# Kernel tuning notes

Hardware: AMD Instinct MI355X
Metric: run time of the kernel (lower is better)

The kernel has to match this reference:

```python
import jax, jax.numpy as jnp
import numpy as np

GROUPS = 16
EPS = 1e-5


def _dcn_v2(x, offset, mask, weight):
    """Modulated deformable 3x3 conv, stride=1, pad=1, no bias.
    x: [B,C,H,W], offset: [B,18,H,W] (dy,dx interleaved per kernel point),
    mask: [B,9,H,W] (modulation scalars), weight: [O,C,3,3]."""
    B, C, H, W = x.shape
    O = weight.shape[0]
    K = 9
    # kernel-point displacements, row-major (kh, kw): k = kh*3 + kw
    ky = jnp.repeat(jnp.arange(3) - 1, 3).astype(x.dtype)   # [9]
    kx = jnp.tile(jnp.arange(3) - 1, 3).astype(x.dtype)      # [9]
    dy = offset[:, 0::2]  # [B,9,H,W]
    dx = offset[:, 1::2]  # [B,9,H,W]
    hh = jnp.arange(H, dtype=x.dtype)
    ww = jnp.arange(W, dtype=x.dtype)
    # sampling coordinates (stride=1, pad=1)
    ys = hh[None, None, :, None] + ky[None, :, None, None] + dy  # [B,9,H,W]
    xs = ww[None, None, None, :] + kx[None, :, None, None] + dx  # [B,9,H,W]

    y0 = jnp.floor(ys)
    x0 = jnp.floor(xs)
    wy1 = ys - y0
    wx1 = xs - x0
    y0i = y0.astype(jnp.int32)
    x0i = x0.astype(jnp.int32)

    flat = x.reshape(B, C, H * W)

    def gather(yi, xi, w):
        # yi, xi, w: [B,9,H,W]; zero-padding outside the image
        valid = (yi >= 0) & (yi < H) & (xi >= 0) & (xi < W)
        idx = jnp.clip(yi, 0, H - 1) * W + jnp.clip(xi, 0, W - 1)  # [B,9,H,W]
        g = jnp.take_along_axis(flat, idx.reshape(B, 1, K * H * W), axis=2)
        g = g.reshape(B, C, K, H, W)
        return g * (w * valid.astype(x.dtype))[:, None]  # [B,C,9,H,W]

    val = (gather(y0i,     x0i,     (1 - wy1) * (1 - wx1))
         + gather(y0i,     x0i + 1, (1 - wy1) * wx1)
         + gather(y0i + 1, x0i,     wy1 * (1 - wx1))
         + gather(y0i + 1, x0i + 1, wy1 * wx1))
    val = val * mask[:, None]  # modulation
    # implicit GEMM: [B,C,9,H,W] x [O,C,9] -> [B,O,H,W]
    return jnp.einsum('bckhw,ock->bohw', val, weight.reshape(O, C, K))


def _group_norm(x, gamma, beta):
    B, C, H, W = x.shape
    xg = x.reshape(B, GROUPS, C // GROUPS, H, W)
    mu = xg.mean(axis=(2, 3, 4), keepdims=True)
    var = xg.var(axis=(2, 3, 4), keepdims=True)
    xn = ((xg - mu) * jax.lax.rsqrt(var + EPS)).reshape(B, C, H, W)
    return xn * gamma[None, :, None, None] + beta[None, :, None, None]


def setup_inputs() -> dict:
    key = jax.random.key(0)
    k1, k2, k3, k4 = jax.random.split(key, 4)
    B, C, O, H, W = 8, 256, 256, 64, 64
    x = jax.random.normal(k1, (B, C, H, W), dtype=jnp.float32)
    offset = jax.random.normal(k2, (B, 18, H, W), dtype=jnp.float32)
    mask = jax.random.uniform(k3, (B, 9, H, W), dtype=jnp.float32)
    weight = jax.random.normal(k4, (O, C, 3, 3), dtype=jnp.float32) * (1.0 / np.sqrt(C * 9))
    gamma = jnp.ones((O,), dtype=jnp.float32)
    beta = jnp.zeros((O,), dtype=jnp.float32)
    return {"x": x, "offset": offset, "mask": mask, "weight": weight,
            "gamma": gamma, "beta": beta}


def reference(x, offset, mask, weight, gamma, beta):
    out = _dcn_v2(x, offset, mask, weight)
    return _group_norm(out, gamma, beta)
```

## Files before the change

kernel.cpp:

```cpp
#include <hip/hip_runtime.h>
#include <stdint.h>


#define B_ 8
#define C_ 256
#define O_ 256
#define H_ 64
#define W_ 64
#define HW_ 4096
#define KTOT 2304
#define GROUPS_ 16
#define EPS_ 1e-5f
#define NSTEP 36
#define VROW 72

typedef float  f32x4  __attribute__((ext_vector_type(4)));
typedef short  short8 __attribute__((ext_vector_type(8)));
typedef unsigned int   u32;
typedef unsigned short u16;

#define XT_BYTES   (B_*HW_*C_*2)
#define WIMG_OFF   XT_BYTES
#define WIMG_BYTES (72*16*64*16)
#define STATS_OFF  (WIMG_OFF + WIMG_BYTES)

__device__ __forceinline__ u32 bf16r(float f) {
    u32 u = __float_as_uint(f);
    return (u + 0x7fffu + ((u >> 16) & 1u)) >> 16;
}
__device__ __forceinline__ u32 pack_bf16x2(float lo, float hi) {
    return bf16r(lo) | (bf16r(hi) << 16);
}
__device__ __forceinline__ u32 pack_perm(float lo, float hi) {
    return __builtin_amdgcn_perm(__float_as_uint(hi), __float_as_uint(lo), 0x07060302u);
}
__device__ __forceinline__ float bflo(u32 u) { return __uint_as_float(u << 16); }
__device__ __forceinline__ float bfhi_f(u32 u) { return __uint_as_float(u); }

__device__ __forceinline__ void barrier_lds() {
    asm volatile("s_waitcnt lgkmcnt(0)\n\ts_barrier" ::: "memory");
}

__global__ void k_prep(const float* __restrict__ x, u16* __restrict__ xt,
                       const float* __restrict__ w, u16* __restrict__ wimg) {
    const int bid = blockIdx.x;
    const int tid = threadIdx.x;
    if (bid < 2048) {
        __shared__ float tile[64][65];
        const int b = bid >> 8, ct = (bid >> 6) & 3, pt = bid & 63;
#pragma unroll
        for (int pass = 0; pass < 4; ++pass) {
            const int r  = (tid >> 4) + pass * 16;
            const int pq = tid & 15;
            const f32x4 v = *(const f32x4*)&x[(((size_t)(b * C_ + ct * 64 + r)) << 12)
                                              + pt * 64 + pq * 4];
            tile[r][pq * 4 + 0] = v.x;
            tile[r][pq * 4 + 1] = v.y;
            tile[r][pq * 4 + 2] = v.z;
            tile[r][pq * 4 + 3] = v.w;
        }
        __syncthreads();
        const int pr = tid >> 2, cg = tid & 3;
        u32 o[8];
#pragma unroll
        for (int j = 0; j < 8; ++j)
            o[j] = pack_bf16x2(tile[cg * 16 + 2 * j][pr], tile[cg * 16 + 2 * j + 1][pr]);
        u16* dst = &xt[(((size_t)b << 12) + pt * 64 + pr) * 256 + ct * 64 + cg * 16];
        *(uint4*)dst       = *(uint4*)&o[0];
        *(uint4*)(dst + 8) = *(uint4*)&o[4];
    } else {
        const int item = (bid - 2048) * 256 + tid;
        if (item < 72 * 1024) {
            const int sub = item >> 10;
            const int idx = item & 1023;
            const int k  = sub >> 3;
            const int c0 = (sub & 7) * 32;
            const int lane = idx & 63;
            const int frag = idx >> 6;
            const int col = lane & 15, quad = lane >> 4;
            const int n = frag * 16 + col;
            const float* src = w + (size_t)n * KTOT + (size_t)(c0 + quad * 8) * 9 + k;
            u32 o[4];
#pragma unroll
            for (int j = 0; j < 4; ++j)
                o[j] = pack_bf16x2(src[(size_t)(2 * j) * 9], src[(size_t)(2 * j + 1) * 9]);
            *(uint4*)&wimg[((size_t)sub * 1024 + idx) * 8] = *(uint4*)o;
        }
    }
}

__device__ __forceinline__ void issue_gather(const u16* __restrict__ cb,
                                             const float* __restrict__ mwp,
                                             const int* __restrict__ mip,
                                             int gpos, uint4 g[8], f32x4& mw) {
    mw = *(const f32x4*)&mwp[gpos * 4];
    const int4 ix = *(const int4*)&mip[gpos * 4];
    const u16* p0 = cb + ix.x;
    const u16* p1 = cb + ix.y;
    const u16* p2 = cb + ix.z;
    const u16* p3 = cb + ix.w;
    g[0] = *(const uint4*)p0; g[1] = *(const uint4*)(p0 + 8);
    g[2] = *(const uint4*)p1; g[3] = *(const uint4*)(p1 + 8);
    g[4] = *(const uint4*)p2; g[5] = *(const uint4*)(p2 + 8);
    g[6] = *(const uint4*)p3; g[7] = *(const uint4*)(p3 + 8);
}

__device__ __forceinline__ void interp_store(const uint4 g[8], f32x4 mw, u16* dst) {
    float s[16];
#pragma unroll
    for (int i = 0; i < 16; ++i) s[i] = 0.f;
    const float ww[4] = {mw.x, mw.y, mw.z, mw.w};
#pragma unroll
    for (int cr = 0; cr < 4; ++cr) {
        const float wg = ww[cr];
        const uint4 a = g[2 * cr], bq = g[2 * cr + 1];
        s[0]  += wg * bflo(a.x);  s[1]  += wg * bfhi_f(a.x);
        s[2]  += wg * bflo(a.y);  s[3]  += wg * bfhi_f(a.y);
        s[4]  += wg * bflo(a.z);  s[5]  += wg * bfhi_f(a.z);
        s[6]  += wg * bflo(a.w);  s[7]  += wg * bfhi_f(a.w);
        s[8]  += wg * bflo(bq.x); s[9]  += wg * bfhi_f(bq.x);
        s[10] += wg * bflo(bq.y); s[11] += wg * bfhi_f(bq.y);
        s[12] += wg * bflo(bq.z); s[13] += wg * bfhi_f(bq.z);
        s[14] += wg * bflo(bq.w); s[15] += wg * bfhi_f(bq.w);
    }
    uint4 pk0, pk1;
    pk0.x = pack_perm(s[0], s[1]);   pk0.y = pack_perm(s[2], s[3]);
    pk0.z = pack_perm(s[4], s[5]);   pk0.w = pack_perm(s[6], s[7]);
    pk1.x = pack_perm(s[8], s[9]);   pk1.y = pack_perm(s[10], s[11]);
    pk1.z = pack_perm(s[12], s[13]); pk1.w = pack_perm(s[14], s[15]);
    *(uint4*)dst = pk0;
    *(uint4*)(dst + 8) = pk1;
}

__device__ __forceinline__ void load_wfrags(const u16* __restrict__ wimg, int s,
                                            int wid, int lane, short8 bf[8]) {
#pragma unroll
    for (int kc = 0; kc < 2; ++kc)
#pragma unroll
        for (int ni = 0; ni < 4; ++ni)
            bf[kc * 4 + ni] = *(const short8*)
                &wimg[(((size_t)(2 * s + kc) * 16 + wid * 4 + ni) * 64 + lane) * 8];
}

__launch_bounds__(256, 2)
__global__ void k_dcn(const u16* __restrict__ xt, const u16* __restrict__ wimg,
                      const float* __restrict__ offp, const float* __restrict__ mskp,
                      float* __restrict__ out, float* __restrict__ stats) {
    __shared__ __align__(16) float meta_w[9 * 64 * 4];
    __shared__ __align__(16) int   meta_i[9 * 64 * 4];
    __shared__ __align__(16) u16   lds_v[2][64 * VROW];

    const int tid = threadIdx.x;
    const int gid = blockIdx.x;
    const int b   = gid & 7;
    const int m0  = (gid >> 3) * 64;
    const int lane = tid & 63, wid = tid >> 6;
    const int col = lane & 15, quad = lane >> 4;
    const int gpos = tid >> 2, oct = tid & 3;

    const u16* xtb = xt + ((size_t)b << 20);

    for (int it = tid; it < 576; it += 256) {
        const int pos = it & 63, k = it >> 6;
        const int pg = m0 + pos;
        const int hh = pg >> 6, wwi = pg & 63;
        const float dy = offp[((size_t)(b * 18 + 2 * k) << 12) + pg];
        const float dx = offp[((size_t)(b * 18 + 2 * k + 1) << 12) + pg];
        const float mv = mskp[((size_t)(b * 9 + k) << 12) + pg];
        const float ys = (float)(hh + (k / 3) - 1) + dy;
        const float xs = (float)(wwi + (k % 3) - 1) + dx;
        const float y0f = floorf(ys), x0f = floorf(xs);
        const int y0 = (int)y0f, x0 = (int)x0f;
        const float wy1 = ys - y0f, wx1 = xs - x0f;
        const float wy0 = 1.f - wy1, wx0 = 1.f - wx1;
        const int y1 = y0 + 1, x1 = x0 + 1;
        const float vy0 = (y0 >= 0 && y0 < H_) ? 1.f : 0.f;
        const float vy1 = (y1 >= 0 && y1 < H_) ? 1.f : 0.f;
        const float vx0 = (x0 >= 0 && x0 < W_) ? 1.f : 0.f;
        const float vx1 = (x1 >= 0 && x1 < W_) ? 1.f : 0.f;
        const int y0c = min(max(y0, 0), H_ - 1), y1c = min(max(y1, 0), H_ - 1);
        const int x0c = min(max(x0, 0), W_ - 1), x1c = min(max(x1, 0), W_ - 1);
        meta_w[it * 4 + 0] = mv * wy0 * wx0 * vy0 * vx0;
        meta_w[it * 4 + 1] = mv * wy0 * wx1 * vy0 * vx1;
        meta_w[it * 4 + 2] = mv * wy1 * wx0 * vy1 * vx0;
        meta_w[it * 4 + 3] = mv * wy1 * wx1 * vy1 * vx1;
        meta_i[it * 4 + 0] = (y0c * W_ + x0c) << 8;
        meta_i[it * 4 + 1] = (y0c * W_ + x1c) << 8;
        meta_i[it * 4 + 2] = (y1c * W_ + x0c) << 8;
        meta_i[it * 4 + 3] = (y1c * W_ + x1c) << 8;
    }
    __syncthreads();

    uint4 g2[2][8]; f32x4 mw2[2]; short8 bf_cur[8], bf_nxt[8];
    issue_gather(xtb + 0 + oct * 16, &meta_w[0], &meta_i[0], gpos, g2[0], mw2[0]);
    load_wfrags(wimg, 0, wid, lane, bf_cur);
    interp_store(g2[0], mw2[0], &lds_v[0][gpos * VROW + oct * 16]);
    issue_gather(xtb + 64 + oct * 16, &meta_w[0], &meta_i[0], gpos, g2[1], mw2[1]);
    __syncthreads();

    f32x4 acc[4][4];
#pragma unroll
    for (int i = 0; i < 4; ++i)
#pragma unroll
        for (int j = 0; j < 4; ++j) acc[i][j] = (f32x4){0.f, 0.f, 0.f, 0.f};

#pragma unroll 2
    for (int s = 0; s < NSTEP; ++s) {
        const int p = s & 1;

        if (s + 1 < NSTEP) load_wfrags(wimg, s + 1, wid, lane, bf_nxt);

        if (s + 2 < NSTEP) {
            const int sn = s + 2;
            const int kn = sn >> 2, c0n = (sn & 3) * 64;
            issue_gather(xtb + c0n + oct * 16, &meta_w[kn * 256], &meta_i[kn * 256],
                         gpos, g2[p], mw2[p]);
        }

#pragma unroll
        for (int kc = 0; kc < 2; ++kc) {
            short8 af[4];
#pragma unroll
            for (int mi = 0; mi < 4; ++mi)
                af[mi] = *(const short8*)
                    &lds_v[p][(mi * 16 + col) * VROW + kc * 32 + quad * 8];
#pragma unroll
            for (int mi = 0; mi < 4; ++mi)
#pragma unroll
                for (int ni = 0; ni < 4; ++ni)
                    acc[mi][ni] = __builtin_amdgcn_mfma_f32_16x16x32_bf16(
                        af[mi], bf_cur[kc * 4 + ni], acc[mi][ni], 0, 0, 0);
        }

        if (s + 1 < NSTEP)
            interp_store(g2[1 - p], mw2[1 - p], &lds_v[1 - p][gpos * VROW + oct * 16]);

        barrier_lds();

#pragma unroll
        for (int j = 0; j < 8; ++j) bf_cur[j] = bf_nxt[j];
    }

#pragma unroll
    for (int mi = 0; mi < 4; ++mi)
#pragma unroll
        for (int ni = 0; ni < 4; ++ni) {
            const int o  = wid * 64 + ni * 16 + col;
            const int pg = m0 + mi * 16 + quad * 4;
            *(f32x4*)(out + (((size_t)b * O_ + o) << 12) + pg) = acc[mi][ni];
        }

#pragma unroll
    for (int ni = 0; ni < 4; ++ni) {
        float s = 0.f, s2 = 0.f;
#pragma unroll
        for (int mi = 0; mi < 4; ++mi) {
            f32x4 v = acc[mi][ni];
            s  += v.x + v.y + v.z + v.w;
            s2 += v.x * v.x + v.y * v.y + v.z * v.z + v.w * v.w;
        }
#pragma unroll
        for (int d = 32; d > 0; d >>= 1) {
            s  += __shfl_xor(s, d, 64);
            s2 += __shfl_xor(s2, d, 64);
        }
        if (lane == 0) {
            const int gI = wid * 4 + ni;
            atomicAdd(&stats[b * GROUPS_ + gI], s);
            atomicAdd(&stats[128 + b * GROUPS_ + gI], s2);
        }
    }
}

__global__ void k_gn(float* __restrict__ out, const float* __restrict__ stats,
                     const float* __restrict__ gamma, const float* __restrict__ beta) {
    const int blk = blockIdx.x;
    const int b = blk >> 8, o = blk & 255;
    const int gI = b * GROUPS_ + (o >> 4);
    const float n = 65536.f;
    const float mean = stats[gI] / n;
    const float var  = stats[128 + gI] / n - mean * mean;
    const float inv  = rsqrtf(fmaxf(var, 0.f) + EPS_);
    const float scale = inv * gamma[o];
    const float shift = beta[o] - mean * scale;
    f32x4* p = (f32x4*)(out + ((size_t)blk << 12));
    const int t = threadIdx.x;
#pragma unroll
    for (int i = 0; i < 4; ++i) {
        f32x4 v = p[t + i * 256];
        p[t + i * 256] = v * scale + shift;
    }
}

extern "C" void kernel_launch(void* const* d_in, const int* in_sizes, int n_in,
                              void* d_out, int out_size, void* d_ws, size_t ws_size,
                              hipStream_t stream) {
    const float* x     = (const float*)d_in[0];
    const float* offp  = (const float*)d_in[1];
    const float* mskp  = (const float*)d_in[2];
    const float* w     = (const float*)d_in[3];
    const float* gamma = (const float*)d_in[4];
    const float* beta  = (const float*)d_in[5];
    float* outp = (float*)d_out;

    u16*   xt    = (u16*)d_ws;
    u16*   wimg  = (u16*)((char*)d_ws + WIMG_OFF);
    float* stats = (float*)((char*)d_ws + STATS_OFF);

    hipMemsetAsync(stats, 0, 1024, stream);
    k_prep<<<dim3(2048 + 288), dim3(256), 0, stream>>>(x, xt, w, wimg);
    k_dcn<<<dim3(512), dim3(256), 0, stream>>>(xt, wimg, offp, mskp, outp, stats);
    k_gn<<<dim3(2048), dim3(256), 0, stream>>>(outp, stats, gamma, beta);
}
```

Before: 185.0 us.

## Double k_dcn block to 512 threads, halve per-thread gather and MFMA work

The DCN kernel now runs 8 waves per block instead of 4. Each wave owns 32 output channels instead of 64, and each thread gathers 8 channels per bilinear corner instead of 16. Weight-fragment prefetching into a second register set is removed, so fragments load at the start of each step, which cuts register pressure so more waves can stay resident to hide gather latency. The separate memset of the statistics buffer is folded into an extra block of the prep kernel, saving one launch. In exchange, weight-load latency is no longer hidden behind the previous step, and the block pays more barrier cost.

Result: faster. 181.2 us (-2.1%).

```diff
diff --git a/kernel.cpp b/kernel.cpp
--- a/kernel.cpp
+++ b/kernel.cpp
@@ -42,9 +42,14 @@
 }
 
 __global__ void k_prep(const float* __restrict__ x, u16* __restrict__ xt,
-                       const float* __restrict__ w, u16* __restrict__ wimg) {
+                       const float* __restrict__ w, u16* __restrict__ wimg,
+                       float* __restrict__ stats) {
     const int bid = blockIdx.x;
     const int tid = threadIdx.x;
+    if (bid >= 2048 + 288) {
+        stats[tid] = 0.f;
+        return;
+    }
     if (bid < 2048) {
         __shared__ float tile[64][65];
         const int b = bid >> 8, ct = (bid >> 6) & 3, pt = bid & 63;
@@ -92,57 +97,48 @@
 __device__ __forceinline__ void issue_gather(const u16* __restrict__ cb,
                                              const float* __restrict__ mwp,
                                              const int* __restrict__ mip,
-                                             int gpos, uint4 g[8], f32x4& mw) {
+                                             int gpos, uint4 g[4], f32x4& mw) {
     mw = *(const f32x4*)&mwp[gpos * 4];
     const int4 ix = *(const int4*)&mip[gpos * 4];
-    const u16* p0 = cb + ix.x;
-    const u16* p1 = cb + ix.y;
-    const u16* p2 = cb + ix.z;
-    const u16* p3 = cb + ix.w;
-    g[0] = *(const uint4*)p0; g[1] = *(const uint4*)(p0 + 8);
-    g[2] = *(const uint4*)p1; g[3] = *(const uint4*)(p1 + 8);
-    g[4] = *(const uint4*)p2; g[5] = *(const uint4*)(p2 + 8);
-    g[6] = *(const uint4*)p3; g[7] = *(const uint4*)(p3 + 8);
-}
-
-__device__ __forceinline__ void interp_store(const uint4 g[8], f32x4 mw, u16* dst) {
-    float s[16];
-#pragma unroll
-    for (int i = 0; i < 16; ++i) s[i] = 0.f;
+    g[0] = *(const uint4*)(cb + ix.x);
+    g[1] = *(const uint4*)(cb + ix.y);
+    g[2] = *(const uint4*)(cb + ix.z);
+    g[3] = *(const uint4*)(cb + ix.w);
+}
+
+__device__ __forceinline__ void interp_store(const uint4 g[4], f32x4 mw, u16* dst) {
+    float s[8];
+#pragma unroll
+    for (int i = 0; i < 8; ++i) s[i] = 0.f;
     const float ww[4] = {mw.x, mw.y, mw.z, mw.w};
 #pragma unroll
     for (int cr = 0; cr < 4; ++cr) {
         const float wg = ww[cr];
-        const uint4 a = g[2 * cr], bq = g[2 * cr + 1];
-        s[0]  += wg * bflo(a.x);  s[1]  += wg * bfhi_f(a.x);
-        s[2]  += wg * bflo(a.y);  s[3]  += wg * bfhi_f(a.y);
-        s[4]  += wg * bflo(a.z);  s[5]  += wg * bfhi_f(a.z);
-        s[6]  += wg * bflo(a.w);  s[7]  += wg * bfhi_f(a.w);
-        s[8]  += wg * bflo(bq.x); s[9]  += wg * bfhi_f(bq.x);
-        s[10] += wg * bflo(bq.y); s[11] += wg * bfhi_f(bq.y);
-        s[12] += wg * bflo(bq.z); s[13] += wg * bfhi_f(bq.z);
-        s[14] += wg * bflo(bq.w); s[15] += wg * bfhi_f(bq.w);
-    }
-    uint4 pk0, pk1;
-    pk0.x = pack_perm(s[0], s[1]);   pk0.y = pack_perm(s[2], s[3]);
-    pk0.z = pack_perm(s[4], s[5]);   pk0.w = pack_perm(s[6], s[7]);
-    pk1.x = pack_perm(s[8], s[9]);   pk1.y = pack_perm(s[10], s[11]);
-    pk1.z = pack_perm(s[12], s[13]); pk1.w = pack_perm(s[14], s[15]);
-    *(uint4*)dst = pk0;
-    *(uint4*)(dst + 8) = pk1;
+        const uint4 a = g[cr];
+        s[0] += wg * bflo(a.x);  s[1] += wg * bfhi_f(a.x);
+        s[2] += wg * bflo(a.y);  s[3] += wg * bfhi_f(a.y);
+        s[4] += wg * bflo(a.z);  s[5] += wg * bfhi_f(a.z);
+        s[6] += wg * bflo(a.w);  s[7] += wg * bfhi_f(a.w);
+    }
+    uint4 pk;
+    pk.x = pack_perm(s[0], s[1]);
+    pk.y = pack_perm(s[2], s[3]);
+    pk.z = pack_perm(s[4], s[5]);
+    pk.w = pack_perm(s[6], s[7]);
+    *(uint4*)dst = pk;
 }
 
 __device__ __forceinline__ void load_wfrags(const u16* __restrict__ wimg, int s,
-                                            int wid, int lane, short8 bf[8]) {
+                                            int wid, int lane, short8 bf[4]) {
 #pragma unroll
     for (int kc = 0; kc < 2; ++kc)
 #pragma unroll
-        for (int ni = 0; ni < 4; ++ni)
-            bf[kc * 4 + ni] = *(const short8*)
-                &wimg[(((size_t)(2 * s + kc) * 16 + wid * 4 + ni) * 64 + lane) * 8];
-}
-
-__launch_bounds__(256, 2)
+        for (int ni = 0; ni < 2; ++ni)
+            bf[kc * 2 + ni] = *(const short8*)
+                &wimg[(((size_t)(2 * s + kc) * 16 + wid * 2 + ni) * 64 + lane) * 8];
+}
+
+__launch_bounds__(512, 4)
 __global__ void k_dcn(const u16* __restrict__ xt, const u16* __restrict__ wimg,
                       const float* __restrict__ offp, const float* __restrict__ mskp,
                       float* __restrict__ out, float* __restrict__ stats) {
@@ -156,11 +152,11 @@
     const int m0  = (gid >> 3) * 64;
     const int lane = tid & 63, wid = tid >> 6;
     const int col = lane & 15, quad = lane >> 4;
-    const int gpos = tid >> 2, oct = tid & 3;
+    const int gpos = tid >> 3, slot = tid & 7;
 
     const u16* xtb = xt + ((size_t)b << 20);
 
-    for (int it = tid; it < 576; it += 256) {
+    for (int it = tid; it < 576; it += 512) {
         const int pos = it & 63, k = it >> 6;
         const int pg = m0 + pos;
         const int hh = pg >> 6, wwi = pg & 63;
@@ -191,29 +187,28 @@
     }
     __syncthreads();
 
-    uint4 g2[2][8]; f32x4 mw2[2]; short8 bf_cur[8], bf_nxt[8];
-    issue_gather(xtb + 0 + oct * 16, &meta_w[0], &meta_i[0], gpos, g2[0], mw2[0]);
-    load_wfrags(wimg, 0, wid, lane, bf_cur);
-    interp_store(g2[0], mw2[0], &lds_v[0][gpos * VROW + oct * 16]);
-    issue_gather(xtb + 64 + oct * 16, &meta_w[0], &meta_i[0], gpos, g2[1], mw2[1]);
+    uint4 g2[2][4]; f32x4 mw2[2]; short8 bf[4];
+    issue_gather(xtb + 0 + slot * 8, &meta_w[0], &meta_i[0], gpos, g2[0], mw2[0]);
+    interp_store(g2[0], mw2[0], &lds_v[0][gpos * VROW + slot * 8]);
+    issue_gather(xtb + 64 + slot * 8, &meta_w[0], &meta_i[0], gpos, g2[1], mw2[1]);
     __syncthreads();
 
-    f32x4 acc[4][4];
+    f32x4 acc[4][2];
 #pragma unroll
     for (int i = 0; i < 4; ++i)
 #pragma unroll
-        for (int j = 0; j < 4; ++j) acc[i][j] = (f32x4){0.f, 0.f, 0.f, 0.f};
+        for (int j = 0; j < 2; ++j) acc[i][j] = (f32x4){0.f, 0.f, 0.f, 0.f};
 
 #pragma unroll 2
     for (int s = 0; s < NSTEP; ++s) {
         const int p = s & 1;
 
-        if (s + 1 < NSTEP) load_wfrags(wimg, s + 1, wid, lane, bf_nxt);
+        load_wfrags(wimg, s, wid, lane, bf);
 
         if (s + 2 < NSTEP) {
             const int sn = s + 2;
             const int kn = sn >> 2, c0n = (sn & 3) * 64;
-            issue_gather(xtb + c0n + oct * 16, &meta_w[kn * 256], &meta_i[kn * 256],
+            issue_gather(xtb + c0n + slot * 8, &meta_w[kn * 256], &meta_i[kn * 256],
                          gpos, g2[p], mw2[p]);
         }
 
@@ -227,31 +222,28 @@
 #pragma unroll
             for (int mi = 0; mi < 4; ++mi)
 #pragma unroll
-                for (int ni = 0; ni < 4; ++ni)
+                for (int ni = 0; ni < 2; ++ni)
                     acc[mi][ni] = __builtin_amdgcn_mfma_f32_16x16x32_bf16(
-                        af[mi], bf_cur[kc * 4 + ni], acc[mi][ni], 0, 0, 0);
+                        af[mi], bf[kc * 2 + ni], acc[mi][ni], 0, 0, 0);
         }
 
         if (s + 1 < NSTEP)
-            interp_store(g2[1 - p], mw2[1 - p], &lds_v[1 - p][gpos * VROW + oct * 16]);
+            interp_store(g2[1 - p], mw2[1 - p], &lds_v[1 - p][gpos * VROW + slot * 8]);
 
         barrier_lds();
-
-#pragma unroll
-        for (int j = 0; j < 8; ++j) bf_cur[j] = bf_nxt[j];
     }
 
 #pragma unroll
     for (int mi = 0; mi < 4; ++mi)
 #pragma unroll
-        for (int ni = 0; ni < 4; ++ni) {
-            const int o  = wid * 64 + ni * 16 + col;
+        for (int ni = 0; ni < 2; ++ni) {
+            const int o  = wid * 32 + ni * 16 + col;
             const int pg = m0 + mi * 16 + quad * 4;
             *(f32x4*)(out + (((size_t)b * O_ + o) << 12) + pg) = acc[mi][ni];
         }
 
 #pragma unroll
-    for (int ni = 0; ni < 4; ++ni) {
+    for (int ni = 0; ni < 2; ++ni) {
         float s = 0.f, s2 = 0.f;
 #pragma unroll
         for (int mi = 0; mi < 4; ++mi) {
@@ -265,7 +257,7 @@
             s2 += __shfl_xor(s2, d, 64);
         }
         if (lane == 0) {
-            const int gI = wid * 4 + ni;
+            const int gI = wid * 2 + ni;
             atomicAdd(&stats[b * GROUPS_ + gI], s);
             atomicAdd(&stats[128 + b * GROUPS_ + gI], s2);
         }
@@ -307,8 +299,7 @@
     u16*   wimg  = (u16*)((char*)d_ws + WIMG_OFF);
     float* stats = (float*)((char*)d_ws + STATS_OFF);
 
-    hipMemsetAsync(stats, 0, 1024, stream);
-    k_prep<<<dim3(2048 + 288), dim3(256), 0, stream>>>(x, xt, w, wimg);
-    k_dcn<<<dim3(512), dim3(256), 0, stream>>>(xt, wimg, offp, mskp, outp, stats);
+    k_prep<<<dim3(2048 + 288 + 1), dim3(256), 0, stream>>>(x, xt, w, wimg, stats);
+    k_dcn<<<dim3(512), dim3(512), 0, stream>>>(xt, wimg, offp, mskp, outp, stats);
     k_gn<<<dim3(2048), dim3(256), 0, stream>>>(outp, stats, gamma, beta);
 }
```

## Split DCN block into producer gather waves and consumer MFMA waves

Applied to the files above, without the earlier changes.

The DCN kernel now launches 512 threads per block. Four waves only gather and bilinearly interpolate samples into the double-buffered LDS tile, while the other four waves load weight fragments and run the MFMA accumulation. This warp specialization is meant to overlap the irregular gather latency with matrix math, in exchange for per-step barriers across twice as many waves and losing the weight-fragment prefetch. Separately, the stats memset is folded into an extra block of the prep kernel to drop one launch.

Result: slower. 222.8 us (+20.4%).

```diff
diff --git a/kernel.cpp b/kernel.cpp
--- a/kernel.cpp
+++ b/kernel.cpp
@@ -42,9 +42,14 @@
 }
 
 __global__ void k_prep(const float* __restrict__ x, u16* __restrict__ xt,
-                       const float* __restrict__ w, u16* __restrict__ wimg) {
+                       const float* __restrict__ w, u16* __restrict__ wimg,
+                       float* __restrict__ stats) {
     const int bid = blockIdx.x;
     const int tid = threadIdx.x;
+    if (bid >= 2048 + 288) {
+        stats[tid] = 0.f;
+        return;
+    }
     if (bid < 2048) {
         __shared__ float tile[64][65];
         const int b = bid >> 8, ct = (bid >> 6) & 3, pt = bid & 63;
@@ -89,12 +94,12 @@
     }
 }
 
-__device__ __forceinline__ void issue_gather(const u16* __restrict__ cb,
-                                             const float* __restrict__ mwp,
-                                             const int* __restrict__ mip,
-                                             int gpos, uint4 g[8], f32x4& mw) {
-    mw = *(const f32x4*)&mwp[gpos * 4];
-    const int4 ix = *(const int4*)&mip[gpos * 4];
+__device__ __forceinline__ void issue_gather16(const u16* __restrict__ cb,
+                                               const float* __restrict__ mwp,
+                                               const int* __restrict__ mip,
+                                               int ppos, uint4 g[8], f32x4& mw) {
+    mw = *(const f32x4*)&mwp[ppos * 4];
+    const int4 ix = *(const int4*)&mip[ppos * 4];
     const u16* p0 = cb + ix.x;
     const u16* p1 = cb + ix.y;
     const u16* p2 = cb + ix.z;
@@ -105,7 +110,7 @@
     g[6] = *(const uint4*)p3; g[7] = *(const uint4*)(p3 + 8);
 }
 
-__device__ __forceinline__ void interp_store(const uint4 g[8], f32x4 mw, u16* dst) {
+__device__ __forceinline__ void interp_store16(const uint4 g[8], f32x4 mw, u16* dst) {
     float s[16];
 #pragma unroll
     for (int i = 0; i < 16; ++i) s[i] = 0.f;
@@ -132,17 +137,7 @@
     *(uint4*)(dst + 8) = pk1;
 }
 
-__device__ __forceinline__ void load_wfrags(const u16* __restrict__ wimg, int s,
-                                            int wid, int lane, short8 bf[8]) {
-#pragma unroll
-    for (int kc = 0; kc < 2; ++kc)
-#pragma unroll
-        for (int ni = 0; ni < 4; ++ni)
-            bf[kc * 4 + ni] = *(const short8*)
-                &wimg[(((size_t)(2 * s + kc) * 16 + wid * 4 + ni) * 64 + lane) * 8];
-}
-
-__launch_bounds__(256, 2)
+__launch_bounds__(512, 2)
 __global__ void k_dcn(const u16* __restrict__ xt, const u16* __restrict__ wimg,
                       const float* __restrict__ offp, const float* __restrict__ mskp,
                       float* __restrict__ out, float* __restrict__ stats) {
@@ -155,12 +150,11 @@
     const int b   = gid & 7;
     const int m0  = (gid >> 3) * 64;
     const int lane = tid & 63, wid = tid >> 6;
-    const int col = lane & 15, quad = lane >> 4;
-    const int gpos = tid >> 2, oct = tid & 3;
+    const bool producer = (wid < 4);
 
     const u16* xtb = xt + ((size_t)b << 20);
 
-    for (int it = tid; it < 576; it += 256) {
+    for (int it = tid; it < 576; it += 512) {
         const int pos = it & 63, k = it >> 6;
         const int pg = m0 + pos;
         const int hh = pg >> 6, wwi = pg & 63;
@@ -191,82 +185,93 @@
     }
     __syncthreads();
 
-    uint4 g2[2][8]; f32x4 mw2[2]; short8 bf_cur[8], bf_nxt[8];
-    issue_gather(xtb + 0 + oct * 16, &meta_w[0], &meta_i[0], gpos, g2[0], mw2[0]);
-    load_wfrags(wimg, 0, wid, lane, bf_cur);
-    interp_store(g2[0], mw2[0], &lds_v[0][gpos * VROW + oct * 16]);
-    issue_gather(xtb + 64 + oct * 16, &meta_w[0], &meta_i[0], gpos, g2[1], mw2[1]);
+    const int ppos = tid >> 2, pslot = tid & 3;
+    const u16* gb = xtb + pslot * 16;
+    u16* wdst0 = &lds_v[0][ppos * VROW + pslot * 16];
+    u16* wdst1 = &lds_v[1][ppos * VROW + pslot * 16];
+    uint4 g2[2][8]; f32x4 mw2[2];
+    const int cw = wid - 4;
+    const int col = lane & 15, quad = lane >> 4;
+    f32x4 acc[4][4];
+
+    if (producer) {
+        issue_gather16(gb, &meta_w[0], &meta_i[0], ppos, g2[0], mw2[0]);
+        interp_store16(g2[0], mw2[0], wdst0);
+        issue_gather16(gb + 64, &meta_w[0], &meta_i[0], ppos, g2[1], mw2[1]);
+    } else {
+#pragma unroll
+        for (int i = 0; i < 4; ++i)
+#pragma unroll
+            for (int j = 0; j < 4; ++j) acc[i][j] = (f32x4){0.f, 0.f, 0.f, 0.f};
+    }
     __syncthreads();
-
-    f32x4 acc[4][4];
-#pragma unroll
-    for (int i = 0; i < 4; ++i)
-#pragma unroll
-        for (int j = 0; j < 4; ++j) acc[i][j] = (f32x4){0.f, 0.f, 0.f, 0.f};
 
 #pragma unroll 2
     for (int s = 0; s < NSTEP; ++s) {
-        const int p = s & 1;
-
-        if (s + 1 < NSTEP) load_wfrags(wimg, s + 1, wid, lane, bf_nxt);
-
-        if (s + 2 < NSTEP) {
-            const int sn = s + 2;
-            const int kn = sn >> 2, c0n = (sn & 3) * 64;
-            issue_gather(xtb + c0n + oct * 16, &meta_w[kn * 256], &meta_i[kn * 256],
-                         gpos, g2[p], mw2[p]);
-        }
-
-#pragma unroll
-        for (int kc = 0; kc < 2; ++kc) {
-            short8 af[4];
-#pragma unroll
-            for (int mi = 0; mi < 4; ++mi)
-                af[mi] = *(const short8*)
-                    &lds_v[p][(mi * 16 + col) * VROW + kc * 32 + quad * 8];
-#pragma unroll
-            for (int mi = 0; mi < 4; ++mi)
+        if (producer) {
+            if (s + 2 < NSTEP) {
+                const int sn = s + 2;
+                issue_gather16(gb + (sn & 3) * 64,
+                               &meta_w[(sn >> 2) * 256], &meta_i[(sn >> 2) * 256],
+                               ppos, g2[s & 1], mw2[s & 1]);
+            }
+            if (s + 1 < NSTEP)
+                interp_store16(g2[(s + 1) & 1], mw2[(s + 1) & 1],
+                               ((s + 1) & 1) ? wdst1 : wdst0);
+        } else {
+            short8 bf[8];
+#pragma unroll
+            for (int kc = 0; kc < 2; ++kc)
 #pragma unroll
                 for (int ni = 0; ni < 4; ++ni)
-                    acc[mi][ni] = __builtin_amdgcn_mfma_f32_16x16x32_bf16(
-                        af[mi], bf_cur[kc * 4 + ni], acc[mi][ni], 0, 0, 0);
-        }
-
-        if (s + 1 < NSTEP)
-            interp_store(g2[1 - p], mw2[1 - p], &lds_v[1 - p][gpos * VROW + oct * 16]);
-
-        barrier_lds();
-
-#pragma unroll
-        for (int j = 0; j < 8; ++j) bf_cur[j] = bf_nxt[j];
-    }
+                    bf[kc * 4 + ni] = *(const short8*)
+                        &wimg[(((size_t)(2 * s + kc) * 16 + cw * 4 + ni) * 64 + lane) * 8];
+#pragma unroll
+            for (int kc = 0; kc < 2; ++kc) {
+                short8 af[4];
+#pragma unroll
+                for (int mi = 0; mi < 4; ++mi)
+                    af[mi] = *(const short8*)
+                        &lds_v[s & 1][(mi * 16 + col) * VROW + kc * 32 + quad * 8];
+#pragma unroll
+                for (int mi = 0; mi < 4; ++mi)
+#pragma unroll
+                    for (int ni = 0; ni < 4; ++ni)
+                        acc[mi][ni] = __builtin_amdgcn_mfma_f32_16x16x32_bf16(
+                            af[mi], bf[kc * 4 + ni], acc[mi][ni], 0, 0, 0);
+            }
+        }
+        if (s + 1 < NSTEP) barrier_lds();
+    }
+
+    if (producer) return;
 
 #pragma unroll
     for (int mi = 0; mi < 4; ++mi)
 #pragma unroll
         for (int ni = 0; ni < 4; ++ni) {
-            const int o  = wid * 64 + ni * 16 + col;
+            const int o  = cw * 64 + ni * 16 + col;
             const int pg = m0 + mi * 16 + quad * 4;
             *(f32x4*)(out + (((size_t)b * O_ + o) << 12) + pg) = acc[mi][ni];
         }
 
 #pragma unroll
     for (int ni = 0; ni < 4; ++ni) {
-        float s = 0.f, s2 = 0.f;
+        float s1 = 0.f, s2 = 0.f;
 #pragma unroll
         for (int mi = 0; mi < 4; ++mi) {
             f32x4 v = acc[mi][ni];
-            s  += v.x + v.y + v.z + v.w;
+            s1 += v.x + v.y + v.z + v.w;
             s2 += v.x * v.x + v.y * v.y + v.z * v.z + v.w * v.w;
         }
 #pragma unroll
         for (int d = 32; d > 0; d >>= 1) {
-            s  += __shfl_xor(s, d, 64);
+            s1 += __shfl_xor(s1, d, 64);
             s2 += __shfl_xor(s2, d, 64);
         }
         if (lane == 0) {
-            const int gI = wid * 4 + ni;
-            atomicAdd(&stats[b * GROUPS_ + gI], s);
+            const int gI = cw * 4 + ni;
+            atomicAdd(&stats[b * GROUPS_ + gI], s1);
             atomicAdd(&stats[128 + b * GROUPS_ + gI], s2);
         }
     }
@@ -307,8 +312,7 @@
     u16*   wimg  = (u16*)((char*)d_ws + WIMG_OFF);
     float* stats = (float*)((char*)d_ws + STATS_OFF);
 
-    hipMemsetAsync(stats, 0, 1024, stream);
-    k_prep<<<dim3(2048 + 288), dim3(256), 0, stream>>>(x, xt, w, wimg);
-    k_dcn<<<dim3(512), dim3(256), 0, stream>>>(xt, wimg, offp, mskp, outp, stats);
+    k_prep<<<dim3(2048 + 288 + 1), dim3(256), 0, stream>>>(x, xt, w, wimg, stats);
+    k_dcn<<<dim3(512), dim3(512), 0, stream>>>(xt, wimg, offp, mskp, outp, stats);
     k_gn<<<dim3(2048), dim3(256), 0, stream>>>(outp, stats, gamma, beta);
 }
```
